# Performance work log

Hardware: AMD Instinct MI355X
Metric: run time of the kernel (lower is better)

The kernel has to match this reference:

```python
import jax, jax.numpy as jnp
import numpy as np

N = 50000      # num nodes
E = 500000     # num edges
IN = 128       # in_dim
H = 8          # num_heads
D = 16         # h_dim (out_dim)
CLAMP = 5.0

def setup_inputs() -> dict:
    key = jax.random.key(0)
    ks = jax.random.split(key, 12)
    def xavier(k, shape, fan_in, fan_out):
        std = float(np.sqrt(2.0 / (fan_in + fan_out)))
        return jax.random.normal(k, shape, dtype=jnp.float32) * std
    return {
        "x": jax.random.normal(ks[0], (N, IN), dtype=jnp.float32),
        "edge_attr": jax.random.normal(ks[1], (E, IN), dtype=jnp.float32),
        "edge_index": jax.random.randint(ks[2], (2, E), 0, N, dtype=jnp.int32),
        # Linear weights stored as [in, out] for x @ W + b
        "WQ": xavier(ks[3], (IN, H * D), IN, H * D),
        "bQ": jnp.zeros((H * D,), jnp.float32),
        "WK": xavier(ks[4], (IN, H * D), IN, H * D),
        "bK": jnp.zeros((H * D,), jnp.float32),
        "WE": xavier(ks[5], (IN, 2 * H * D), IN, 2 * H * D),
        "bE": jnp.zeros((2 * H * D,), jnp.float32),
        "WV": xavier(ks[6], (IN, H * D), IN, H * D),
        "bV": jnp.zeros((H * D,), jnp.float32),
        "Aw": xavier(ks[7], (D, H, 1), D, 1),
        "VeRow": xavier(ks[8], (D, H, D), D, D),
    }

def reference(x, edge_attr, edge_index, WQ, bQ, WK, bK, WE, bE, WV, bV, Aw, VeRow):
    src, dst = edge_index[0], edge_index[1]
    Qh = (x @ WQ + bQ).reshape(N, H, D)
    Kh = (x @ WK + bK).reshape(N, H, D)
    Vh = (x @ WV + bV).reshape(N, H, D)
    Ex = (edge_attr @ WE + bE).reshape(E, H, 2 * D)

    # additive score: gathered K/Q plus signed-sqrt edge term
    score1 = Kh[src] + Qh[dst]                       # [E,H,D]
    s2 = Ex[:, :, :D] * Ex[:, :, D:]
    score2 = jnp.sqrt(jax.nn.relu(s2)) - jnp.sqrt(jax.nn.relu(-s2))
    conn = score1 + score2                           # act = Identity

    score = jnp.einsum('ehd,dhc->ehc', conn, Aw)     # [E,H,1]
    score = jnp.clip(score, -CLAMP, CLAMP)

    # scatter-softmax over destination nodes
    m = jax.ops.segment_max(score, dst, num_segments=N)      # [N,H,1]
    ex = jnp.exp(score - m[dst])
    denom = jax.ops.segment_sum(ex, dst, num_segments=N)
    attn = ex / (denom[dst] + 1e-16)                 # [E,H,1]

    # weighted scatter-add aggregation
    msg = Vh[src] * attn                             # [E,H,D]
    Vo = Qh + jax.ops.segment_sum(msg, dst, num_segments=N)
    rowV = jax.ops.segment_sum(conn * attn, dst, num_segments=N)
    Vo = Vo + jnp.einsum('nhd,dhc->nhc', rowV, VeRow)

    return Vo.reshape(N, H * D), conn.reshape(E, H * D)
```

## Files before the change

### kernel.cpp

```cpp
#include <hip/hip_runtime.h>
#include <math.h>

#define N_NODES 50000
#define N_EDGES 500000
#define IN_DIM  128
#define NH      8
#define HD      16
#define OUTD    128
#define CLAMP_V 5.0f

__global__ __launch_bounds__(256) void node_gemm_kernel(
    const float* __restrict__ x,
    const float* __restrict__ WQ, const float* __restrict__ bQ,
    const float* __restrict__ WK, const float* __restrict__ bK,
    const float* __restrict__ WV, const float* __restrict__ bV,
    float* __restrict__ Vo, float* __restrict__ Kh, float* __restrict__ Vh)
{
    __shared__ float A[64][132];
    __shared__ float B[64][64];

    const int t  = threadIdx.x;
    const int bx = blockIdx.x;
    const int by = blockIdx.y;
    const int which = by >> 1;
    const int ch    = (by & 1) * 64;

    const float* W    = (which == 0) ? WQ : (which == 1 ? WK : WV);
    const float* bias = (which == 0) ? bQ : (which == 1 ? bK : bV);
    float*       out  = (which == 0) ? Vo : (which == 1 ? Kh : Vh);

    const int r0 = bx * 64;

    #pragma unroll
    for (int it = 0; it < 8; ++it) {
        int idx = it * 256 + t;
        int k4  = idx & 31;
        int r   = idx >> 5;
        float4 v = make_float4(0.f, 0.f, 0.f, 0.f);
        if (r0 + r < N_NODES)
            v = *(const float4*)(x + (size_t)(r0 + r) * IN_DIM + k4 * 4);
        *(float4*)&A[r][k4 * 4] = v;
    }

    const int tx = t & 15, ty = t >> 4;
    float acc[4][4] = {};

    for (int kh = 0; kh < 2; ++kh) {
        __syncthreads();
        #pragma unroll
        for (int it = 0; it < 4; ++it) {
            int idx = it * 256 + t;
            int c4  = idx & 15;
            int kk  = idx >> 4;
            float4 v = *(const float4*)(W + (size_t)(kh * 64 + kk) * 128 + ch + c4 * 4);
            *(float4*)&B[kk][c4 * 4] = v;
        }
        __syncthreads();

        #pragma unroll 4
        for (int k = 0; k < 64; k += 4) {
            float4 a4[4], b4[4];
            a4[0] = *(const float4*)&A[ty * 4 + 0][kh * 64 + k];
            a4[1] = *(const float4*)&A[ty * 4 + 1][kh * 64 + k];
            a4[2] = *(const float4*)&A[ty * 4 + 2][kh * 64 + k];
            a4[3] = *(const float4*)&A[ty * 4 + 3][kh * 64 + k];
            b4[0] = *(const float4*)&B[k + 0][tx * 4];
            b4[1] = *(const float4*)&B[k + 1][tx * 4];
            b4[2] = *(const float4*)&B[k + 2][tx * 4];
            b4[3] = *(const float4*)&B[k + 3][tx * 4];
            const float* aa = (const float*)a4;
            const float* bb = (const float*)b4;
            #pragma unroll
            for (int kk = 0; kk < 4; ++kk)
                #pragma unroll
                for (int i = 0; i < 4; ++i)
                    #pragma unroll
                    for (int j = 0; j < 4; ++j)
                        acc[i][j] += aa[i * 4 + kk] * bb[kk * 4 + j];
        }
    }

    #pragma unroll
    for (int i = 0; i < 4; ++i) {
        int r = r0 + ty * 4 + i;
        if (r < N_NODES) {
            #pragma unroll
            for (int j = 0; j < 4; ++j) {
                int c = ch + tx * 4 + j;
                out[(size_t)r * OUTD + c] = acc[i][j] + bias[c];
            }
        }
    }
}

__global__ __launch_bounds__(256) void edge_kernel(
    const float* __restrict__ edge_attr,
    const int*   __restrict__ edge_index,
    const float* __restrict__ WE, const float* __restrict__ bE,
    const float* __restrict__ Aw,
    const float* __restrict__ Qh,
    const float* __restrict__ Kh,
    float* __restrict__ conn_out,
    float* __restrict__ exp_s,
    float* __restrict__ denom)
{
    __shared__ float A[64][132];
    __shared__ float B[64][64];

    const int t  = threadIdx.x;
    const int e0 = blockIdx.x * 64;
    const int c0 = blockIdx.y * 64;

    #pragma unroll
    for (int it = 0; it < 8; ++it) {
        int idx = it * 256 + t;
        int k4  = idx & 31;
        int r   = idx >> 5;
        float4 v = make_float4(0.f, 0.f, 0.f, 0.f);
        if (e0 + r < N_EDGES)
            v = *(const float4*)(edge_attr + (size_t)(e0 + r) * IN_DIM + k4 * 4);
        *(float4*)&A[r][k4 * 4] = v;
    }

    const int tx = t & 15, ty = t >> 4;
    float acc[4][4] = {};

    for (int kh = 0; kh < 2; ++kh) {
        __syncthreads();
        #pragma unroll
        for (int it = 0; it < 4; ++it) {
            int idx = it * 256 + t;
            int c4  = idx & 15;
            int kk  = idx >> 4;
            float4 v = *(const float4*)(WE + (size_t)(kh * 64 + kk) * 256 + c0 + c4 * 4);
            *(float4*)&B[kk][c4 * 4] = v;
        }
        __syncthreads();

        #pragma unroll 4
        for (int k = 0; k < 64; k += 4) {
            float4 a4[4], b4[4];
            a4[0] = *(const float4*)&A[ty * 4 + 0][kh * 64 + k];
            a4[1] = *(const float4*)&A[ty * 4 + 1][kh * 64 + k];
            a4[2] = *(const float4*)&A[ty * 4 + 2][kh * 64 + k];
            a4[3] = *(const float4*)&A[ty * 4 + 3][kh * 64 + k];
            b4[0] = *(const float4*)&B[k + 0][tx * 4];
            b4[1] = *(const float4*)&B[k + 1][tx * 4];
            b4[2] = *(const float4*)&B[k + 2][tx * 4];
            b4[3] = *(const float4*)&B[k + 3][tx * 4];
            const float* aa = (const float*)a4;
            const float* bb = (const float*)b4;
            #pragma unroll
            for (int kk = 0; kk < 4; ++kk)
                #pragma unroll
                for (int i = 0; i < 4; ++i)
                    #pragma unroll
                    for (int j = 0; j < 4; ++j)
                        acc[i][j] += aa[i * 4 + kk] * bb[kk * 4 + j];
        }
    }
    __syncthreads();

    #pragma unroll
    for (int i = 0; i < 4; ++i)
        #pragma unroll
        for (int j = 0; j < 4; ++j)
            A[ty * 4 + i][tx * 4 + j] = acc[i][j] + bE[c0 + tx * 4 + j];
    __syncthreads();

    if (t < 128) {
        const int r  = t >> 1;
        const int hl = t & 1;
        const int e  = e0 + r;
        if (e < N_EDGES) {
            const int h   = (c0 >> 5) + hl;
            const int src = edge_index[e];
            const int dst = edge_index[N_EDGES + e];

            const float4* K4 = (const float4*)(Kh + (size_t)src * OUTD + h * HD);
            const float4* Q4 = (const float4*)(Qh + (size_t)dst * OUTD + h * HD);
            float kq[16];
            #pragma unroll
            for (int i = 0; i < 4; ++i) {
                float4 kk = K4[i], qq = Q4[i];
                kq[i * 4 + 0] = kk.x + qq.x;
                kq[i * 4 + 1] = kk.y + qq.y;
                kq[i * 4 + 2] = kk.z + qq.z;
                kq[i * 4 + 3] = kk.w + qq.w;
            }

            float cv[16];
            float score = 0.f;
            #pragma unroll
            for (int d = 0; d < 16; ++d) {
                float s2 = A[r][hl * 32 + d] * A[r][hl * 32 + 16 + d];
                float sq = (s2 >= 0.f) ? sqrtf(s2) : -sqrtf(-s2);
                float c  = kq[d] + sq;
                cv[d] = c;
                score += c * Aw[d * NH + h];
            }
            float4* co = (float4*)(conn_out + (size_t)e * OUTD + h * HD);
            #pragma unroll
            for (int i = 0; i < 4; ++i)
                co[i] = make_float4(cv[i * 4 + 0], cv[i * 4 + 1],
                                    cv[i * 4 + 2], cv[i * 4 + 3]);

            score = fminf(fmaxf(score, -CLAMP_V), CLAMP_V);
            float ex = expf(score);
            exp_s[(size_t)e * NH + h] = ex;
            atomicAdd(&denom[(size_t)dst * NH + h], ex);
        }
    }
}

__global__ __launch_bounds__(256) void scatter_kernel(
    const int*   __restrict__ edge_index,
    const float* __restrict__ Vh,
    const float* __restrict__ conn,
    const float* __restrict__ exp_s,
    const float* __restrict__ denom,
    float* __restrict__ Vo,
    float* __restrict__ rowV)
{
    const int t = threadIdx.x;
    const int e = blockIdx.x * 2 + (t >> 7);
    const int c = t & 127;
    const int h = c >> 4;

    const int src = edge_index[e];
    const int dst = edge_index[N_EDGES + e];

    const float attn = exp_s[(size_t)e * NH + h] /
                       (denom[(size_t)dst * NH + h] + 1e-16f);

    const float mv = Vh[(size_t)src * OUTD + c] * attn;
    atomicAdd(&Vo[(size_t)dst * OUTD + c], mv);
    const float rv = conn[(size_t)e * OUTD + c] * attn;
    atomicAdd(&rowV[(size_t)dst * OUTD + c], rv);
}

__global__ __launch_bounds__(256) void finalize_kernel(
    const float* __restrict__ rowV,
    const float* __restrict__ VeRow,
    float* __restrict__ Vo)
{
    __shared__ float ver[2048];
    __shared__ float rv[256];
    const int t = threadIdx.x;

    #pragma unroll
    for (int it = 0; it < 2; ++it) {
        int idx = it * 256 + t;
        *(float4*)&ver[idx * 4] = *(const float4*)&VeRow[idx * 4];
    }
    const int n0 = blockIdx.x * 2;
    if (t < 64)
        *(float4*)&rv[t * 4] = *(const float4*)&rowV[(size_t)n0 * OUTD + t * 4];
    __syncthreads();

    const int nl = t >> 7, c = t & 127, h = c >> 4, cc = c & 15;
    float acc = 0.f;
    #pragma unroll
    for (int d = 0; d < 16; ++d)
        acc += rv[nl * 128 + h * 16 + d] * ver[d * 128 + h * 16 + cc];

    Vo[(size_t)(n0 + nl) * OUTD + c] += acc;
}

extern "C" void kernel_launch(void* const* d_in, const int* in_sizes, int n_in,
                              void* d_out, int out_size, void* d_ws, size_t ws_size,
                              hipStream_t stream)
{
    const float* x         = (const float*)d_in[0];
    const float* edge_attr = (const float*)d_in[1];
    const int*   edge_index= (const int*)  d_in[2];
    const float* WQ = (const float*)d_in[3];
    const float* bQ = (const float*)d_in[4];
    const float* WK = (const float*)d_in[5];
    const float* bK = (const float*)d_in[6];
    const float* WE = (const float*)d_in[7];
    const float* bE = (const float*)d_in[8];
    const float* WV = (const float*)d_in[9];
    const float* bV = (const float*)d_in[10];
    const float* Aw = (const float*)d_in[11];
    const float* VeRow = (const float*)d_in[12];

    float* Vo   = (float*)d_out;
    float* conn = Vo + (size_t)N_NODES * OUTD;

    float* ws    = (float*)d_ws;
    float* Kh    = ws;
    float* Vh    = Kh   + (size_t)N_NODES * OUTD;
    float* rowV  = Vh   + (size_t)N_NODES * OUTD;
    float* denom = rowV + (size_t)N_NODES * OUTD;
    float* exp_s = denom+ (size_t)N_NODES * NH;

    hipMemsetAsync(rowV,  0, (size_t)N_NODES * OUTD * sizeof(float), stream);
    hipMemsetAsync(denom, 0, (size_t)N_NODES * NH   * sizeof(float), stream);

    dim3 g1((N_NODES + 63) / 64, 6);
    node_gemm_kernel<<<g1, 256, 0, stream>>>(x, WQ, bQ, WK, bK, WV, bV, Vo, Kh, Vh);

    dim3 g2((N_EDGES + 63) / 64, 4);
    edge_kernel<<<g2, 256, 0, stream>>>(edge_attr, edge_index, WE, bE, Aw,
                                        Vo, Kh, conn, exp_s, denom);

    scatter_kernel<<<N_EDGES / 2, 256, 0, stream>>>(edge_index, Vh, conn,
                                                    exp_s, denom, Vo, rowV);

    finalize_kernel<<<N_NODES / 2, 256, 0, stream>>>(rowV, VeRow, Vo);
}
```

Baseline: 1.550 ms.

## Compute edge projection GEMM with split-bf16 MFMA instead of FP32 FMAs

The edge-attribute projection now runs on MFMA bf16 instructions. Both operands are split into hi and lo bf16 parts, and three products are summed to keep close to FP32 accuracy. WE is pre-packed and transposed into a temporary buffer at the end of the rowV workspace, so the rowV memset moves after the edge kernel. Tiles grow to 128 edges by 128 columns with swizzled LDS, which cuts redundant edge_attr loads across column blocks. The split-precision scheme adds conversion work and drops the lo*lo term, so results can differ slightly from FP32.

```diff
diff --git a/kernel.cpp b/kernel.cpp
--- a/kernel.cpp
+++ b/kernel.cpp
@@ -8,6 +8,31 @@
 #define HD      16
 #define OUTD    128
 #define CLAMP_V 5.0f
+
+typedef unsigned short ushort_t;
+typedef short bf16x8 __attribute__((ext_vector_type(8)));
+typedef float f32x16 __attribute__((ext_vector_type(16)));
+
+__device__ __forceinline__ ushort_t f2bf(float f) {
+    uint32_t u = __float_as_uint(f);
+    u += 0x7fffu + ((u >> 16) & 1u);
+    return (ushort_t)(u >> 16);
+}
+__device__ __forceinline__ float bf2f(ushort_t h) {
+    return __uint_as_float(((uint32_t)h) << 16);
+}
+
+__global__ __launch_bounds__(256) void pack_we_kernel(
+    const float* __restrict__ WE,
+    ushort_t* __restrict__ hi, ushort_t* __restrict__ lo)
+{
+    int idx = blockIdx.x * 256 + threadIdx.x;
+    int n = idx & 255, k = idx >> 8;
+    float v = WE[(size_t)k * 256 + n];
+    ushort_t h = f2bf(v);
+    hi[(size_t)n * 128 + k] = h;
+    lo[(size_t)n * 128 + k] = f2bf(v - bf2f(h));
+}
 
 __global__ __launch_bounds__(256) void node_gemm_kernel(
     const float* __restrict__ x,
@@ -96,7 +121,9 @@
 __global__ __launch_bounds__(256) void edge_kernel(
     const float* __restrict__ edge_attr,
     const int*   __restrict__ edge_index,
-    const float* __restrict__ WE, const float* __restrict__ bE,
+    const ushort_t* __restrict__ WEt_hi,
+    const ushort_t* __restrict__ WEt_lo,
+    const float* __restrict__ bE,
     const float* __restrict__ Aw,
     const float* __restrict__ Qh,
     const float* __restrict__ Kh,
@@ -104,78 +131,115 @@
     float* __restrict__ exp_s,
     float* __restrict__ denom)
 {
-    __shared__ float A[64][132];
-    __shared__ float B[64][64];
-
-    const int t  = threadIdx.x;
-    const int e0 = blockIdx.x * 64;
-    const int c0 = blockIdx.y * 64;
-
-    #pragma unroll
-    for (int it = 0; it < 8; ++it) {
-        int idx = it * 256 + t;
-        int k4  = idx & 31;
-        int r   = idx >> 5;
-        float4 v = make_float4(0.f, 0.f, 0.f, 0.f);
-        if (e0 + r < N_EDGES)
-            v = *(const float4*)(edge_attr + (size_t)(e0 + r) * IN_DIM + k4 * 4);
-        *(float4*)&A[r][k4 * 4] = v;
-    }
-
-    const int tx = t & 15, ty = t >> 4;
-    float acc[4][4] = {};
-
+    __shared__ ushort_t u16[32768];
+
+    const int t   = threadIdx.x;
+    const int bid = blockIdx.x;
+    const int et  = bid >> 1;
+    const int ch  = bid & 1;
+    const int e0  = et * 128;
+    const int c0  = ch * 128;
+
+    const int lane = t & 63;
+    const int w    = t >> 6;
+    const int we   = w >> 1;
+    const int wc   = w & 1;
+
+    f32x16 acc[2][2];
+    #pragma unroll
+    for (int i = 0; i < 2; ++i)
+        #pragma unroll
+        for (int j = 0; j < 2; ++j)
+            #pragma unroll
+            for (int rgi = 0; rgi < 16; ++rgi)
+                acc[i][j][rgi] = 0.f;
+
+    #pragma unroll
     for (int kh = 0; kh < 2; ++kh) {
         __syncthreads();
         #pragma unroll
+        for (int it = 0; it < 8; ++it) {
+            int idx = it * 256 + t;
+            int k4  = idx & 15;
+            int r   = idx >> 4;
+            float4 v = make_float4(0.f, 0.f, 0.f, 0.f);
+            if (e0 + r < N_EDGES)
+                v = *(const float4*)(edge_attr + (size_t)(e0 + r) * IN_DIM + kh * 64 + k4 * 4);
+            ushort_t ha = f2bf(v.x), hb = f2bf(v.y), hc = f2bf(v.z), hd = f2bf(v.w);
+            ushort_t la = f2bf(v.x - bf2f(ha)), lb = f2bf(v.y - bf2f(hb)),
+                     lc = f2bf(v.z - bf2f(hc)), ld = f2bf(v.w - bf2f(hd));
+            int off = r * 64 + ((k4 * 4) ^ ((r & 7) << 3));
+            *(uint2*)&u16[off]        = make_uint2((uint32_t)ha | ((uint32_t)hb << 16),
+                                                   (uint32_t)hc | ((uint32_t)hd << 16));
+            *(uint2*)&u16[8192 + off] = make_uint2((uint32_t)la | ((uint32_t)lb << 16),
+                                                   (uint32_t)lc | ((uint32_t)ld << 16));
+        }
+        #pragma unroll
         for (int it = 0; it < 4; ++it) {
             int idx = it * 256 + t;
-            int c4  = idx & 15;
-            int kk  = idx >> 4;
-            float4 v = *(const float4*)(WE + (size_t)(kh * 64 + kk) * 256 + c0 + c4 * 4);
-            *(float4*)&B[kk][c4 * 4] = v;
+            int kc  = idx & 7;
+            int c   = idx >> 3;
+            size_t goff = (size_t)(c0 + c) * 128 + kh * 64 + kc * 8;
+            int off = c * 64 + ((kc * 8) ^ ((c & 7) << 3));
+            *(uint4*)&u16[16384 + off] = *(const uint4*)&WEt_hi[goff];
+            *(uint4*)&u16[24576 + off] = *(const uint4*)&WEt_lo[goff];
         }
         __syncthreads();
 
-        #pragma unroll 4
-        for (int k = 0; k < 64; k += 4) {
-            float4 a4[4], b4[4];
-            a4[0] = *(const float4*)&A[ty * 4 + 0][kh * 64 + k];
-            a4[1] = *(const float4*)&A[ty * 4 + 1][kh * 64 + k];
-            a4[2] = *(const float4*)&A[ty * 4 + 2][kh * 64 + k];
-            a4[3] = *(const float4*)&A[ty * 4 + 3][kh * 64 + k];
-            b4[0] = *(const float4*)&B[k + 0][tx * 4];
-            b4[1] = *(const float4*)&B[k + 1][tx * 4];
-            b4[2] = *(const float4*)&B[k + 2][tx * 4];
-            b4[3] = *(const float4*)&B[k + 3][tx * 4];
-            const float* aa = (const float*)a4;
-            const float* bb = (const float*)b4;
-            #pragma unroll
-            for (int kk = 0; kk < 4; ++kk)
+        #pragma unroll
+        for (int ks = 0; ks < 4; ++ks) {
+            const int kloc = ks * 16 + ((lane >> 5) << 3);
+            bf16x8 eh[2], el[2], wh2[2], wl2[2];
+            #pragma unroll
+            for (int f = 0; f < 2; ++f) {
+                int er = we * 64 + f * 32 + (lane & 31);
+                int eo = er * 64 + (kloc ^ ((er & 7) << 3));
+                eh[f] = *(bf16x8*)&u16[eo];
+                el[f] = *(bf16x8*)&u16[8192 + eo];
+                int cr = wc * 64 + f * 32 + (lane & 31);
+                int co = cr * 64 + (kloc ^ ((cr & 7) << 3));
+                wh2[f] = *(bf16x8*)&u16[16384 + co];
+                wl2[f] = *(bf16x8*)&u16[24576 + co];
+            }
+            #pragma unroll
+            for (int i = 0; i < 2; ++i)
                 #pragma unroll
-                for (int i = 0; i < 4; ++i)
-                    #pragma unroll
-                    for (int j = 0; j < 4; ++j)
-                        acc[i][j] += aa[i * 4 + kk] * bb[kk * 4 + j];
+                for (int j = 0; j < 2; ++j) {
+                    acc[i][j] = __builtin_amdgcn_mfma_f32_32x32x16_bf16(eh[i], wh2[j], acc[i][j], 0, 0, 0);
+                    acc[i][j] = __builtin_amdgcn_mfma_f32_32x32x16_bf16(eh[i], wl2[j], acc[i][j], 0, 0, 0);
+                    acc[i][j] = __builtin_amdgcn_mfma_f32_32x32x16_bf16(el[i], wh2[j], acc[i][j], 0, 0, 0);
+                }
         }
     }
     __syncthreads();
 
-    #pragma unroll
-    for (int i = 0; i < 4; ++i)
-        #pragma unroll
-        for (int j = 0; j < 4; ++j)
-            A[ty * 4 + i][tx * 4 + j] = acc[i][j] + bE[c0 + tx * 4 + j];
+    float* stash = (float*)u16;
+    {
+        float bj[2];
+        bj[0] = bE[c0 + wc * 64 + 0  + (lane & 31)];
+        bj[1] = bE[c0 + wc * 64 + 32 + (lane & 31)];
+        #pragma unroll
+        for (int i = 0; i < 2; ++i)
+            #pragma unroll
+            for (int j = 0; j < 2; ++j)
+                #pragma unroll
+                for (int rgi = 0; rgi < 16; ++rgi) {
+                    int r = we * 64 + i * 32 + (rgi & 3) + 8 * (rgi >> 2) + 4 * (lane >> 5);
+                    int c = wc * 64 + j * 32 + (lane & 31);
+                    stash[r * 128 + c] = acc[i][j][rgi] + bj[j];
+                }
+    }
     __syncthreads();
 
-    if (t < 128) {
-        const int r  = t >> 1;
-        const int hl = t & 1;
-        const int e  = e0 + r;
-        if (e < N_EDGES) {
-            const int h   = (c0 >> 5) + hl;
-            const int src = edge_index[e];
-            const int dst = edge_index[N_EDGES + e];
+    const int r = t >> 1;
+    const int e = e0 + r;
+    if (e < N_EDGES) {
+        const int src = edge_index[e];
+        const int dst = edge_index[N_EDGES + e];
+        #pragma unroll
+        for (int hh = 0; hh < 2; ++hh) {
+            const int hl = (t & 1) + hh * 2;
+            const int h  = ch * 4 + hl;
 
             const float4* K4 = (const float4*)(Kh + (size_t)src * OUTD + h * HD);
             const float4* Q4 = (const float4*)(Qh + (size_t)dst * OUTD + h * HD);
@@ -193,7 +257,7 @@
             float score = 0.f;
             #pragma unroll
             for (int d = 0; d < 16; ++d) {
-                float s2 = A[r][hl * 32 + d] * A[r][hl * 32 + 16 + d];
+                float s2 = stash[r * 128 + hl * 32 + d] * stash[r * 128 + hl * 32 + 16 + d];
                 float sq = (s2 >= 0.f) ? sqrtf(s2) : -sqrtf(-s2);
                 float c  = kq[d] + sq;
                 cv[d] = c;
@@ -295,15 +359,21 @@
     float* denom = rowV + (size_t)N_NODES * OUTD;
     float* exp_s = denom+ (size_t)N_NODES * NH;
 
-    hipMemsetAsync(rowV,  0, (size_t)N_NODES * OUTD * sizeof(float), stream);
-    hipMemsetAsync(denom, 0, (size_t)N_NODES * NH   * sizeof(float), stream);
+    ushort_t* WEt_hi = (ushort_t*)(rowV + (size_t)N_NODES * OUTD - 32768);
+    ushort_t* WEt_lo = WEt_hi + 32768;
+
+    hipMemsetAsync(denom, 0, (size_t)N_NODES * NH * sizeof(float), stream);
+
+    pack_we_kernel<<<128, 256, 0, stream>>>(WE, WEt_hi, WEt_lo);
 
     dim3 g1((N_NODES + 63) / 64, 6);
     node_gemm_kernel<<<g1, 256, 0, stream>>>(x, WQ, bQ, WK, bK, WV, bV, Vo, Kh, Vh);
 
-    dim3 g2((N_EDGES + 63) / 64, 4);
-    edge_kernel<<<g2, 256, 0, stream>>>(edge_attr, edge_index, WE, bE, Aw,
-                                        Vo, Kh, conn, exp_s, denom);
+    const int nt = (N_EDGES + 127) / 128;
+    edge_kernel<<<nt * 2, 256, 0, stream>>>(edge_attr, edge_index, WEt_hi, WEt_lo,
+                                            bE, Aw, Vo, Kh, conn, exp_s, denom);
+
+    hipMemsetAsync(rowV, 0, (size_t)N_NODES * OUTD * sizeof(float), stream);
 
     scatter_kernel<<<N_EDGES / 2, 256, 0, stream>>>(edge_index, Vh, conn,
                                                     exp_s, denom, Vo, rowV);
```

Measured after the change: 1.284 ms. 1.21x faster.
